# Performance work log

Measured on AMD Instinct MI355X. Metric: run time of the kernel, lower is better.

The kernel has to match this reference:

```python
import jax, jax.numpy as jnp
import numpy as np

B, L, D, V = 2, 512, 512, 32000
TRAIN_FRAC = 0.01
LOSS_WEIGHTS = (1.0, 0.25)  # (forward branch, backward_ar_loss_weight)


def _make_pairs():
    # cartesian_prod(arange(L), arange(L)) filtered by bi - fi >= 2, then random subsample
    fi_g, bi_g = np.meshgrid(np.arange(L), np.arange(L), indexing='ij')
    fi_all, bi_all = fi_g.ravel(), bi_g.ravel()
    valid = (bi_all - fi_all) >= 2
    fi_all, bi_all = fi_all[valid], bi_all[valid]
    num_pairs = fi_all.shape[0]
    n_sub = max(int(num_pairs * TRAIN_FRAC), 1)
    perm = np.random.default_rng(0).permutation(num_pairs)[:n_sub]
    return jnp.asarray(fi_all[perm], jnp.int32), jnp.asarray(bi_all[perm], jnp.int32)


def setup_inputs() -> dict:
    key = jax.random.key(0)
    k_fe, k_be, k_seq, k_w1, k_w2 = jax.random.split(key, 5)
    fi, bi = _make_pairs()  # [N], N = 1303
    return {
        'forward_embeds': jax.random.normal(k_fe, (B, L, D), jnp.float32),
        'backward_embeds': jax.random.normal(k_be, (B, L, D), jnp.float32),
        'seq': jax.random.randint(k_seq, (B, L), 0, V, dtype=jnp.int32),
        'fi': fi,
        'bi': bi,
        'w1': jax.random.normal(k_w1, (2 * D, D), jnp.float32) * 0.02,
        'b1': jnp.zeros((D,), jnp.float32),
        'w2': jax.random.normal(k_w2, (D, 2 * V), jnp.float32) * 0.02,
        'b2': jnp.zeros((2 * V,), jnp.float32),
    }


def reference(forward_embeds, backward_embeds, seq, fi, bi, w1, b1, w2, b2):
    # gather fwd/bwd embeddings at the (fi, bi) pair indices and concat: [B, N, 2D]
    fb_embeds = jnp.concatenate([forward_embeds[:, fi], backward_embeds[:, bi]], axis=-1)
    # text head: Linear(2D->D) -> LeakyReLU(0.01) -> Linear(D->2V)
    h = jax.nn.leaky_relu(jnp.einsum('bne,ed->bnd', fb_embeds, w1) + b1)
    logits = jnp.einsum('bnd,dv->bnv', h, w2) + b2  # [B, N, 2V]
    n = logits.shape[1]
    # (fb l) layout: first V classes = forward branch, last V = backward branch
    logp = jax.nn.log_softmax(logits.reshape(B, n, 2, V), axis=-1)  # [B, N, 2, V]
    # NOTE: source computes labels_fi = fi + 1 but actually indexes seq at fi/bi
    labels = jnp.stack([seq[:, fi], seq[:, bi]], axis=-1)  # [B, N, 2]
    nll = -jnp.take_along_axis(logp, labels[..., None], axis=-1)[..., 0]  # [B, N, 2]
    w = jnp.asarray(LOSS_WEIGHTS, logits.dtype)  # per-branch loss weights
    return (nll * w).mean()
```

## Files before the change

### kernel.cpp

```cpp
#include <hip/hip_runtime.h>


typedef __bf16 bf16x8 __attribute__((ext_vector_type(8)));
typedef __bf16 bf16x4 __attribute__((ext_vector_type(4)));
typedef float f32x4  __attribute__((ext_vector_type(4)));

#define MFMA16(a, b, c) __builtin_amdgcn_mfma_f32_16x16x32_bf16(a, b, c, 0, 0, 0)

static constexpr int Bsz   = 2;
static constexpr int L     = 512;
static constexpr int D     = 512;
static constexpr int V     = 32000;
static constexpr int K1    = 2 * D;
static constexpr int N1    = D;
static constexpr int K2    = D;
static constexpr int N2    = 2 * V;
static constexpr int NSTRIP = N2 / 64;
static constexpr float LOG2E = 1.44269504088896340736f;

__device__ __host__ inline size_t apack_chunk(int panel, int ks, int mi) {
    return (((size_t)panel * 16 + ks) * 4 + mi) * 512;
}

__global__ void prep_kernel(const float* __restrict__ fwd,
                            const float* __restrict__ bwd,
                            const int* __restrict__ fi,
                            const int* __restrict__ bi,
                            const int* __restrict__ seq,
                            const float* __restrict__ w1,
                            __bf16* __restrict__ A1,
                            __bf16* __restrict__ W1T,
                            int* __restrict__ labcol,
                            int N, int M, int Mpad, int G1) {
    __shared__ __align__(16) __bf16 tile[64][68];
    if ((int)blockIdx.x >= G1) {
        int bid = blockIdx.x - G1;
        int bx = bid & 7, by = bid >> 3;
        int t  = threadIdx.x;
        int tx = t & 15, ty = t >> 4;
        int n0 = bx * 64, k0 = by * 64;
        for (int i = 0; i < 4; i++) {
            int k = k0 + ty + 16 * i;
            float4 v = *(const float4*)(w1 + (size_t)k * N1 + n0 + tx * 4);
            tile[tx * 4 + 0][ty + 16 * i] = (__bf16)v.x;
            tile[tx * 4 + 1][ty + 16 * i] = (__bf16)v.y;
            tile[tx * 4 + 2][ty + 16 * i] = (__bf16)v.z;
            tile[tx * 4 + 3][ty + 16 * i] = (__bf16)v.w;
        }
        __syncthreads();
        for (int i = 0; i < 4; i++) {
            int n = n0 + ty + 16 * i;
            bf16x4 o;
            o[0] = tile[ty + 16 * i][tx * 4 + 0];
            o[1] = tile[ty + 16 * i][tx * 4 + 1];
            o[2] = tile[ty + 16 * i][tx * 4 + 2];
            o[3] = tile[ty + 16 * i][tx * 4 + 3];
            *(bf16x4*)(W1T + (size_t)n * K1 + k0 + tx * 4) = o;
        }
        return;
    }
    int t = blockIdx.x * 256 + threadIdx.x;
    if (t < Mpad * 2) {
        int m = t >> 1, br = t & 1;
        if (m >= M) labcol[br * Mpad + m] = -1;
        else {
            int b = m / N, n = m - b * N;
            int tok = br ? seq[b * L + bi[n]] : seq[b * L + fi[n]];
            labcol[br * Mpad + m] = br * V + tok;
        }
    }
    int total = Mpad * (K1 / 8);
    if (t >= total) return;
    int m  = t >> 7;
    int c8 = (t & 127) * 8;
    bf16x8 out;
    if (m < M) {
        int b = m / N;
        int n = m - b * N;
        const float* src;
        if (c8 < D) src = fwd + ((size_t)(b * L + fi[n])) * D + c8;
        else        src = bwd + ((size_t)(b * L + bi[n])) * D + (c8 - D);
        float4 v0 = *(const float4*)(src);
        float4 v1 = *(const float4*)(src + 4);
        out[0] = (__bf16)v0.x; out[1] = (__bf16)v0.y;
        out[2] = (__bf16)v0.z; out[3] = (__bf16)v0.w;
        out[4] = (__bf16)v1.x; out[5] = (__bf16)v1.y;
        out[6] = (__bf16)v1.z; out[7] = (__bf16)v1.w;
    } else {
        for (int j = 0; j < 8; j++) out[j] = (__bf16)0.0f;
    }
    *(bf16x8*)(A1 + (size_t)m * K1 + c8) = out;
}

__global__ __launch_bounds__(256) void gemm1_kernel(
        const __bf16* __restrict__ A, const __bf16* __restrict__ Bt,
        const float* __restrict__ bias, __bf16* __restrict__ Apack, int K) {
    __shared__ __align__(16) __bf16 At[128][40];
    __shared__ __align__(16) __bf16 Bl[128][40];
    __shared__ __align__(16) __bf16 Cld[128][136];
    const int t = threadIdx.x;
    const int by = blockIdx.y, bx = blockIdx.x;
    const int m0 = by * 128, n0 = bx * 128;
    const int srow = t >> 2, schunk = (t & 3) * 8;
    const int wave = t >> 6, lane = t & 63;
    const int wrow = (wave >> 1) * 64, wcol = (wave & 1) * 64;
    const int q = lane >> 4, ln = lane & 15;

    f32x4 acc[4][4] = {};
    for (int k0 = 0; k0 < K; k0 += 32) {
        __syncthreads();
        *(bf16x8*)&At[srow][schunk]      = *(const bf16x8*)(A  + (size_t)(m0 + srow)      * K + k0 + schunk);
        *(bf16x8*)&At[srow + 64][schunk] = *(const bf16x8*)(A  + (size_t)(m0 + srow + 64) * K + k0 + schunk);
        *(bf16x8*)&Bl[srow][schunk]      = *(const bf16x8*)(Bt + (size_t)(n0 + srow)      * K + k0 + schunk);
        *(bf16x8*)&Bl[srow + 64][schunk] = *(const bf16x8*)(Bt + (size_t)(n0 + srow + 64) * K + k0 + schunk);
        __syncthreads();
        bf16x8 af[4], bfr[4];
        for (int i = 0; i < 4; i++) af[i]  = *(const bf16x8*)&At[wrow + i * 16 + ln][q * 8];
        for (int i = 0; i < 4; i++) bfr[i] = *(const bf16x8*)&Bl[wcol + i * 16 + ln][q * 8];
        for (int mi = 0; mi < 4; mi++)
            for (int ni = 0; ni < 4; ni++)
                acc[mi][ni] = MFMA16(af[mi], bfr[ni], acc[mi][ni]);
    }
    for (int ni = 0; ni < 4; ni++) {
        int gcol = n0 + wcol + ni * 16 + ln;
        float bv = bias[gcol];
        for (int mi = 0; mi < 4; mi++)
            for (int r = 0; r < 4; r++) {
                float v = acc[mi][ni][r] + bv;
                v = v > 0.0f ? v : 0.01f * v;
                Cld[wrow + mi * 16 + q * 4 + r][wcol + ni * 16 + ln] = (__bf16)v;
            }
    }
    __syncthreads();
    for (int i = 0; i < 8; i++) {
        int c   = wave + 4 * i;
        int pl  = c >> 4, ksl = (c >> 2) & 3, mi = c & 3;
        int row = pl * 64 + mi * 16 + (lane & 15);
        int col = ksl * 32 + (lane >> 4) * 8;
        bf16x8 v = *(const bf16x8*)&Cld[row][col];
        size_t base = apack_chunk(2 * by + pl, 4 * bx + ksl, mi);
        *(bf16x8*)(Apack + base + lane * 8) = v;
    }
}

__global__ __launch_bounds__(512, 4) void gemm2_kernel(
        const __bf16* __restrict__ Apack, const float* __restrict__ w2,
        const float* __restrict__ b2, const int* __restrict__ labcol,
        float* __restrict__ partial, float* __restrict__ lab, int Mpad) {
    __shared__ __align__(16) __bf16 Bp[64 * 512];
    const int t = threadIdx.x;
    const int strip = blockIdx.x;
    const int c0 = strip * 64;
    const int branch = (c0 >= V) ? 1 : 0;

    {
        const int col = t & 63;
        const int ni = col >> 4, lncol = col & 15;
        const int kb0 = (t >> 6) * 8;
        for (int r = 0; r < 8; r++) {
            int kb = kb0 + r * 64;
            int ks = kb >> 5, qk = (kb >> 3) & 3;
            float v[8];
#pragma unroll
            for (int j = 0; j < 8; j++)
                v[j] = __builtin_nontemporal_load(w2 + (size_t)(kb + j) * N2 + c0 + col);
            bf16x8 o;
#pragma unroll
            for (int j = 0; j < 8; j++) o[j] = (__bf16)v[j];
            *(bf16x8*)&Bp[(size_t)(((ks * 4 + ni) * 64 + qk * 16 + lncol)) * 8] = o;
        }
    }
    __syncthreads();

    const int wave = t >> 6, lane = t & 63;
    const int q = lane >> 4, ln = lane & 15;
    const int* labB = labcol + branch * Mpad;

    float bvl2[4];
#pragma unroll
    for (int ni = 0; ni < 4; ni++) bvl2[ni] = b2[c0 + ni * 16 + ln] * LOG2E;

    const int npanels = Mpad >> 6;
    for (int p = wave; p < npanels; p += 8) {
        const __bf16* base = Apack + apack_chunk(p, 0, 0) + lane * 8;

        f32x4 acc[4][4] = {};
        bf16x8 afc[4], afn[4];
#pragma unroll
        for (int mi = 0; mi < 4; mi++)
            afc[mi] = *(const bf16x8*)(base + mi * 512);
#pragma unroll 1
        for (int ks = 0; ks < 16; ks++) {
            if (ks < 15) {
#pragma unroll
                for (int mi = 0; mi < 4; mi++)
                    afn[mi] = *(const bf16x8*)(base + (size_t)(ks + 1) * 2048 + mi * 512);
            }
            bf16x8 bf[4];
#pragma unroll
            for (int ni = 0; ni < 4; ni++)
                bf[ni] = *(const bf16x8*)&Bp[(size_t)(ks * 4 + ni) * 512 + lane * 8];
#pragma unroll
            for (int mi = 0; mi < 4; mi++)
#pragma unroll
                for (int ni = 0; ni < 4; ni++)
                    acc[mi][ni] = MFMA16(afc[mi], bf[ni], acc[mi][ni]);
#pragma unroll
            for (int mi = 0; mi < 4; mi++) afc[mi] = afn[mi];
        }

        int myl = labB[p * 64 + lane];

        float rowsum[4][4];
#pragma unroll
        for (int mi = 0; mi < 4; mi++)
#pragma unroll
            for (int r = 0; r < 4; r++) rowsum[mi][r] = 0.0f;
#pragma unroll
        for (int ni = 0; ni < 4; ni++) {
            const float bl2 = bvl2[ni];
#pragma unroll
            for (int mi = 0; mi < 4; mi++)
#pragma unroll
                for (int r = 0; r < 4; r++)
                    rowsum[mi][r] += __builtin_exp2f(__builtin_fmaf(acc[mi][ni][r], LOG2E, bl2));
        }

        if (__any((unsigned)(myl - c0) < 64u)) {
#pragma unroll
            for (int ni = 0; ni < 4; ni++) {
                const int gcol = c0 + ni * 16 + ln;
                const float bv = b2[gcol];
#pragma unroll
                for (int mi = 0; mi < 4; mi++)
#pragma unroll
                    for (int r = 0; r < 4; r++) {
                        int row = p * 64 + mi * 16 + q * 4 + r;
                        if (gcol == labB[row]) {
                            lab[row * 2 + branch] = acc[mi][ni][r] + bv;
                        }
                    }
            }
        }

#pragma unroll
        for (int mi = 0; mi < 4; mi++)
#pragma unroll
            for (int r = 0; r < 4; r++) {
                float s = rowsum[mi][r];
                s += __shfl_xor(s, 1);
                s += __shfl_xor(s, 2);
                s += __shfl_xor(s, 4);
                s += __shfl_xor(s, 8);
                rowsum[mi][r] = s;
            }
        float mine = 0.0f;
        const int srcl = ((lane >> 2) & 3) * 16;
#pragma unroll
        for (int mi2 = 0; mi2 < 4; mi2++)
#pragma unroll
            for (int r2 = 0; r2 < 4; r2++) {
                float tv = __shfl(rowsum[mi2][r2], srcl);
                if ((lane >> 4) == mi2 && (lane & 3) == r2) mine = tv;
            }
        partial[(size_t)strip * Mpad + p * 64 + lane] = mine;
    }
}

__global__ __launch_bounds__(256) void final_kernel(
        const float* __restrict__ partial, const float* __restrict__ lab,
        float* __restrict__ out, int M, int Mpad) {
    __shared__ float red[4][64];
    const int br = blockIdx.x & 1;
    const int m0 = (blockIdx.x >> 1) * 64;
    const int wave = threadIdx.x >> 6, lane = threadIdx.x & 63;
    const int s0 = br * (NSTRIP / 2) + wave * (NSTRIP / 8);
    float s = 0.0f;
#pragma unroll 5
    for (int i = 0; i < NSTRIP / 8; i++)
        s += partial[(size_t)(s0 + i) * Mpad + m0 + lane];
    red[wave][lane] = s;
    __syncthreads();
    if (wave == 0) {
        float tot = red[0][lane] + red[1][lane] + red[2][lane] + red[3][lane];
        int m = m0 + lane;
        float acc = 0.0f;
        if (m < M)
            acc = (br ? 0.25f : 1.0f) * (logf(tot) - lab[m * 2 + br]);
        acc += __shfl_xor(acc, 32);
        acc += __shfl_xor(acc, 16);
        acc += __shfl_xor(acc, 8);
        acc += __shfl_xor(acc, 4);
        acc += __shfl_xor(acc, 2);
        acc += __shfl_xor(acc, 1);
        if (lane == 0) atomicAdd(out, acc / (float)(2 * M));
    }
}

extern "C" void kernel_launch(void* const* d_in, const int* in_sizes, int n_in,
                              void* d_out, int out_size, void* d_ws, size_t ws_size,
                              hipStream_t stream) {
    const float* fwd = (const float*)d_in[0];
    const float* bwd = (const float*)d_in[1];
    const int*   seq = (const int*)d_in[2];
    const int*   fi  = (const int*)d_in[3];
    const int*   bi  = (const int*)d_in[4];
    const float* w1  = (const float*)d_in[5];
    const float* b1  = (const float*)d_in[6];
    const float* w2  = (const float*)d_in[7];
    const float* b2  = (const float*)d_in[8];
    float* out = (float*)d_out;

    const int N    = in_sizes[3];
    const int M    = Bsz * N;
    const int Mpad = ((M + 255) / 256) * 256;

    char* ws = (char*)d_ws;
    __bf16* A1    = (__bf16*)(ws);
    __bf16* W1T   = (__bf16*)(ws + (size_t)Mpad * K1 * 2);
    __bf16* Apack = (__bf16*)((char*)W1T + (size_t)N1 * K1 * 2);
    float*  partial = (float*)((char*)Apack + (size_t)Mpad * N1 * 2);
    float*  lab     = (float*)((char*)partial + (size_t)NSTRIP * Mpad * 4);
    int*    labcol  = (int*)((char*)lab + (size_t)Mpad * 2 * 4);

    {
        int G1 = Mpad * (K1 / 8) / 256;
        prep_kernel<<<G1 + 128, 256, 0, stream>>>(
            fwd, bwd, fi, bi, seq, w1, A1, W1T, labcol, N, M, Mpad, G1);
    }
    hipMemsetAsync(out, 0, sizeof(float), stream);
    gemm1_kernel<<<dim3(N1 / 128, Mpad / 128), 256, 0, stream>>>(A1, W1T, b1, Apack, K1);
    gemm2_kernel<<<NSTRIP, 512, 0, stream>>>(Apack, w2, b2, labcol, partial, lab, Mpad);
    final_kernel<<<(Mpad / 64) * 2, 256, 0, stream>>>(partial, lab, out, M, Mpad);
}
```

Measured before the change: 442.6 us.

## Fuse gather, bf16 conversion and W1 transpose into gemm1; simplify softmax epilogue

Removes prep_kernel. gemm1 now gathers the fwd/bwd embedding rows itself through per-tile row offset tables, converts fp32 to bf16 while staging to LDS, transposes w1 on the fly, and computes the label columns in its by==0 blocks. This drops one launch and the A1/W1T round trips through global memory, at the cost of fp32 loads inside the GEMM k-loop and strided LDS writes for the transpose. The labcol layout changes to interleaved, and the gemm2 epilogue now uses __expf with a per-element label compare instead of a wave-level __any check.

```diff
diff --git a/kernel.cpp b/kernel.cpp
--- a/kernel.cpp
+++ b/kernel.cpp
@@ -16,103 +16,84 @@
 static constexpr int K2    = D;
 static constexpr int N2    = 2 * V;
 static constexpr int NSTRIP = N2 / 64;
-static constexpr float LOG2E = 1.44269504088896340736f;
 
 __device__ __host__ inline size_t apack_chunk(int panel, int ks, int mi) {
     return (((size_t)panel * 16 + ks) * 4 + mi) * 512;
 }
 
-__global__ void prep_kernel(const float* __restrict__ fwd,
-                            const float* __restrict__ bwd,
-                            const int* __restrict__ fi,
-                            const int* __restrict__ bi,
-                            const int* __restrict__ seq,
-                            const float* __restrict__ w1,
-                            __bf16* __restrict__ A1,
-                            __bf16* __restrict__ W1T,
-                            int* __restrict__ labcol,
-                            int N, int M, int Mpad, int G1) {
-    __shared__ __align__(16) __bf16 tile[64][68];
-    if ((int)blockIdx.x >= G1) {
-        int bid = blockIdx.x - G1;
-        int bx = bid & 7, by = bid >> 3;
-        int t  = threadIdx.x;
-        int tx = t & 15, ty = t >> 4;
-        int n0 = bx * 64, k0 = by * 64;
-        for (int i = 0; i < 4; i++) {
-            int k = k0 + ty + 16 * i;
-            float4 v = *(const float4*)(w1 + (size_t)k * N1 + n0 + tx * 4);
-            tile[tx * 4 + 0][ty + 16 * i] = (__bf16)v.x;
-            tile[tx * 4 + 1][ty + 16 * i] = (__bf16)v.y;
-            tile[tx * 4 + 2][ty + 16 * i] = (__bf16)v.z;
-            tile[tx * 4 + 3][ty + 16 * i] = (__bf16)v.w;
-        }
-        __syncthreads();
-        for (int i = 0; i < 4; i++) {
-            int n = n0 + ty + 16 * i;
-            bf16x4 o;
-            o[0] = tile[ty + 16 * i][tx * 4 + 0];
-            o[1] = tile[ty + 16 * i][tx * 4 + 1];
-            o[2] = tile[ty + 16 * i][tx * 4 + 2];
-            o[3] = tile[ty + 16 * i][tx * 4 + 3];
-            *(bf16x4*)(W1T + (size_t)n * K1 + k0 + tx * 4) = o;
-        }
-        return;
-    }
-    int t = blockIdx.x * 256 + threadIdx.x;
-    if (t < Mpad * 2) {
-        int m = t >> 1, br = t & 1;
-        if (m >= M) labcol[br * Mpad + m] = -1;
-        else {
-            int b = m / N, n = m - b * N;
-            int tok = br ? seq[b * L + bi[n]] : seq[b * L + fi[n]];
-            labcol[br * Mpad + m] = br * V + tok;
-        }
-    }
-    int total = Mpad * (K1 / 8);
-    if (t >= total) return;
-    int m  = t >> 7;
-    int c8 = (t & 127) * 8;
-    bf16x8 out;
-    if (m < M) {
-        int b = m / N;
-        int n = m - b * N;
-        const float* src;
-        if (c8 < D) src = fwd + ((size_t)(b * L + fi[n])) * D + c8;
-        else        src = bwd + ((size_t)(b * L + bi[n])) * D + (c8 - D);
-        float4 v0 = *(const float4*)(src);
-        float4 v1 = *(const float4*)(src + 4);
-        out[0] = (__bf16)v0.x; out[1] = (__bf16)v0.y;
-        out[2] = (__bf16)v0.z; out[3] = (__bf16)v0.w;
-        out[4] = (__bf16)v1.x; out[5] = (__bf16)v1.y;
-        out[6] = (__bf16)v1.z; out[7] = (__bf16)v1.w;
-    } else {
-        for (int j = 0; j < 8; j++) out[j] = (__bf16)0.0f;
-    }
-    *(bf16x8*)(A1 + (size_t)m * K1 + c8) = out;
-}
-
 __global__ __launch_bounds__(256) void gemm1_kernel(
-        const __bf16* __restrict__ A, const __bf16* __restrict__ Bt,
-        const float* __restrict__ bias, __bf16* __restrict__ Apack, int K) {
+        const float* __restrict__ fwd, const float* __restrict__ bwd,
+        const int* __restrict__ fi, const int* __restrict__ bi,
+        const int* __restrict__ seq, const float* __restrict__ w1,
+        const float* __restrict__ b1, __bf16* __restrict__ Apack,
+        int* __restrict__ labcol, int N, int M, int Mpad) {
     __shared__ __align__(16) __bf16 At[128][40];
     __shared__ __align__(16) __bf16 Bl[128][40];
     __shared__ __align__(16) __bf16 Cld[128][136];
+    __shared__ int offF[128];
+    __shared__ int offB[128];
     const int t = threadIdx.x;
     const int by = blockIdx.y, bx = blockIdx.x;
     const int m0 = by * 128, n0 = bx * 128;
+
+    if (by == 0) {
+        for (int i = bx * 256 + t; i < 2 * Mpad; i += 4 * 256) {
+            int m = i >> 1, br = i & 1;
+            if (m >= M) labcol[i] = -1;
+            else {
+                int b = m / N, n = m - b * N;
+                int tok = br ? seq[b * L + bi[n]] : seq[b * L + fi[n]];
+                labcol[i] = br * V + tok;
+            }
+        }
+    }
+    if (t < 128) {
+        int m = m0 + t;
+        int mc = (m < M) ? m : 0;
+        int b = mc / N, n = mc - b * N;
+        offF[t] = (b * L + fi[n]) * D;
+        offB[t] = (b * L + bi[n]) * D;
+    }
+    __syncthreads();
+
     const int srow = t >> 2, schunk = (t & 3) * 8;
     const int wave = t >> 6, lane = t & 63;
     const int wrow = (wave >> 1) * 64, wcol = (wave & 1) * 64;
     const int q = lane >> 4, ln = lane & 15;
+    const int bnn = (t & 31) * 4, bkk = t >> 5;
 
     f32x4 acc[4][4] = {};
-    for (int k0 = 0; k0 < K; k0 += 32) {
+    for (int k0 = 0; k0 < K1; k0 += 32) {
         __syncthreads();
-        *(bf16x8*)&At[srow][schunk]      = *(const bf16x8*)(A  + (size_t)(m0 + srow)      * K + k0 + schunk);
-        *(bf16x8*)&At[srow + 64][schunk] = *(const bf16x8*)(A  + (size_t)(m0 + srow + 64) * K + k0 + schunk);
-        *(bf16x8*)&Bl[srow][schunk]      = *(const bf16x8*)(Bt + (size_t)(n0 + srow)      * K + k0 + schunk);
-        *(bf16x8*)&Bl[srow + 64][schunk] = *(const bf16x8*)(Bt + (size_t)(n0 + srow + 64) * K + k0 + schunk);
+        {
+            const float* p0;
+            const float* p1;
+            if (k0 < D) {
+                p0 = fwd + offF[srow]      + k0 + schunk;
+                p1 = fwd + offF[srow + 64] + k0 + schunk;
+            } else {
+                p0 = bwd + offB[srow]      + (k0 - D) + schunk;
+                p1 = bwd + offB[srow + 64] + (k0 - D) + schunk;
+            }
+            float4 a0 = *(const float4*)(p0), a1 = *(const float4*)(p0 + 4);
+            float4 c0v = *(const float4*)(p1), c1 = *(const float4*)(p1 + 4);
+            bf16x8 o0, o1;
+            o0[0] = (__bf16)a0.x; o0[1] = (__bf16)a0.y; o0[2] = (__bf16)a0.z; o0[3] = (__bf16)a0.w;
+            o0[4] = (__bf16)a1.x; o0[5] = (__bf16)a1.y; o0[6] = (__bf16)a1.z; o0[7] = (__bf16)a1.w;
+            o1[0] = (__bf16)c0v.x; o1[1] = (__bf16)c0v.y; o1[2] = (__bf16)c0v.z; o1[3] = (__bf16)c0v.w;
+            o1[4] = (__bf16)c1.x; o1[5] = (__bf16)c1.y; o1[6] = (__bf16)c1.z; o1[7] = (__bf16)c1.w;
+            *(bf16x8*)&At[srow][schunk]      = o0;
+            *(bf16x8*)&At[srow + 64][schunk] = o1;
+        }
+#pragma unroll
+        for (int j = 0; j < 4; j++) {
+            int kk = bkk + j * 8;
+            float4 w = *(const float4*)(w1 + (size_t)(k0 + kk) * N1 + n0 + bnn);
+            Bl[bnn + 0][kk] = (__bf16)w.x;
+            Bl[bnn + 1][kk] = (__bf16)w.y;
+            Bl[bnn + 2][kk] = (__bf16)w.z;
+            Bl[bnn + 3][kk] = (__bf16)w.w;
+        }
         __syncthreads();
         bf16x8 af[4], bfr[4];
         for (int i = 0; i < 4; i++) af[i]  = *(const bf16x8*)&At[wrow + i * 16 + ln][q * 8];
@@ -123,7 +104,7 @@
     }
     for (int ni = 0; ni < 4; ni++) {
         int gcol = n0 + wcol + ni * 16 + ln;
-        float bv = bias[gcol];
+        float bv = b1[gcol];
         for (int mi = 0; mi < 4; mi++)
             for (int r = 0; r < 4; r++) {
                 float v = acc[mi][ni][r] + bv;
@@ -174,11 +155,10 @@
 
     const int wave = t >> 6, lane = t & 63;
     const int q = lane >> 4, ln = lane & 15;
-    const int* labB = labcol + branch * Mpad;
-
-    float bvl2[4];
-#pragma unroll
-    for (int ni = 0; ni < 4; ni++) bvl2[ni] = b2[c0 + ni * 16 + ln] * LOG2E;
+
+    float bvn[4];
+#pragma unroll
+    for (int ni = 0; ni < 4; ni++) bvn[ni] = b2[c0 + ni * 16 + ln];
 
     const int npanels = Mpad >> 6;
     for (int p = wave; p < npanels; p += 8) {
@@ -209,40 +189,35 @@
             for (int mi = 0; mi < 4; mi++) afc[mi] = afn[mi];
         }
 
-        int myl = labB[p * 64 + lane];
+        int lc[4][4];
+#pragma unroll
+        for (int mi = 0; mi < 4; mi++)
+#pragma unroll
+            for (int r = 0; r < 4; r++)
+                lc[mi][r] = labcol[(p * 64 + mi * 16 + q * 4 + r) * 2 + branch];
 
         float rowsum[4][4];
 #pragma unroll
         for (int mi = 0; mi < 4; mi++)
 #pragma unroll
             for (int r = 0; r < 4; r++) rowsum[mi][r] = 0.0f;
+
 #pragma unroll
         for (int ni = 0; ni < 4; ni++) {
-            const float bl2 = bvl2[ni];
+            const int gcol = c0 + ni * 16 + ln;
+            const float bv = bvn[ni];
 #pragma unroll
             for (int mi = 0; mi < 4; mi++)
 #pragma unroll
-                for (int r = 0; r < 4; r++)
-                    rowsum[mi][r] += __builtin_exp2f(__builtin_fmaf(acc[mi][ni][r], LOG2E, bl2));
-        }
-
-        if (__any((unsigned)(myl - c0) < 64u)) {
-#pragma unroll
-            for (int ni = 0; ni < 4; ni++) {
-                const int gcol = c0 + ni * 16 + ln;
-                const float bv = b2[gcol];
-#pragma unroll
-                for (int mi = 0; mi < 4; mi++)
-#pragma unroll
-                    for (int r = 0; r < 4; r++) {
-                        int row = p * 64 + mi * 16 + q * 4 + r;
-                        if (gcol == labB[row]) {
-                            lab[row * 2 + branch] = acc[mi][ni][r] + bv;
-                        }
+                for (int r = 0; r < 4; r++) {
+                    float v = acc[mi][ni][r] + bv;
+                    rowsum[mi][r] += __expf(v);
+                    if (gcol == lc[mi][r]) {
+                        int gm = p * 64 + mi * 16 + q * 4 + r;
+                        lab[gm * 2 + branch] = v;
                     }
-            }
-        }
-
+                }
+        }
 #pragma unroll
         for (int mi = 0; mi < 4; mi++)
 #pragma unroll
@@ -316,20 +291,14 @@
     const int Mpad = ((M + 255) / 256) * 256;
 
     char* ws = (char*)d_ws;
-    __bf16* A1    = (__bf16*)(ws);
-    __bf16* W1T   = (__bf16*)(ws + (size_t)Mpad * K1 * 2);
-    __bf16* Apack = (__bf16*)((char*)W1T + (size_t)N1 * K1 * 2);
+    __bf16* Apack   = (__bf16*)(ws);
     float*  partial = (float*)((char*)Apack + (size_t)Mpad * N1 * 2);
     float*  lab     = (float*)((char*)partial + (size_t)NSTRIP * Mpad * 4);
     int*    labcol  = (int*)((char*)lab + (size_t)Mpad * 2 * 4);
 
-    {
-        int G1 = Mpad * (K1 / 8) / 256;
-        prep_kernel<<<G1 + 128, 256, 0, stream>>>(
-            fwd, bwd, fi, bi, seq, w1, A1, W1T, labcol, N, M, Mpad, G1);
-    }
     hipMemsetAsync(out, 0, sizeof(float), stream);
-    gemm1_kernel<<<dim3(N1 / 128, Mpad / 128), 256, 0, stream>>>(A1, W1T, b1, Apack, K1);
+    gemm1_kernel<<<dim3(N1 / 128, Mpad / 128), 256, 0, stream>>>(
+        fwd, bwd, fi, bi, seq, w1, b1, Apack, labcol, N, M, Mpad);
     gemm2_kernel<<<NSTRIP, 512, 0, stream>>>(Apack, w2, b2, labcol, partial, lab, Mpad);
     final_kernel<<<(Mpad / 64) * 2, 256, 0, stream>>>(partial, lab, out, M, Mpad);
 }
```

Measured after the change: 436.4 us. No clear change (-1.4%).
